# Performance work log

Measured on AMD Instinct MI355X. Metric: run time of the kernel, lower is better.

## Reference

```python
import jax, jax.numpy as jnp
import numpy as np

B, S, D, K = 64, 512, 512, 1024
DECAY = 0.99
EPS = 1e-05
COMMITMENT_COST = 0.25
PAD_IDX = 0


def setup_inputs() -> dict:
    key = jax.random.key(0)
    k1, k2, k3 = jax.random.split(key, 3)
    inputs = jax.random.normal(k1, (B, S, D), dtype=jnp.float32)
    padding_mask = jax.random.bernoulli(k2, 0.1, (B, S))
    codebook_w = jax.random.normal(k3, (K, D), dtype=jnp.float32) * 0.02
    codebook_w = codebook_w.at[PAD_IDX].set(0.0)  # padding_idx row zeroed
    ema_cluster_size = jnp.zeros((K,), dtype=jnp.float32)
    ema_w = codebook_w  # _ema_w initialized as copy of codebook
    return {"inputs": inputs, "padding_mask": padding_mask,
            "codebook_w": codebook_w, "ema_cluster_size": ema_cluster_size,
            "ema_w": ema_w}


def reference(inputs, padding_mask, codebook_w, ema_cluster_size, ema_w):
    input_shape = inputs.shape
    flat = inputs.reshape(-1, D)                      # [N, D]
    mask = padding_mask.reshape(-1)                   # [N], True = pad

    # squared euclidean distances: [N, K]
    dist = (jnp.sum(flat * flat, axis=1, keepdims=True)
            + jnp.sum(codebook_w * codebook_w, axis=1)
            - 2.0 * flat @ codebook_w.T)
    # non-padded tokens cannot pick code 0; padded tokens must pick code 0
    inf = jnp.float32(np.inf)
    col0 = jnp.where(mask, dist[:, 0], inf)
    rest = jnp.where(mask[:, None], inf, dist[:, 1:])
    dist = jnp.concatenate([col0[:, None], rest], axis=1)

    idx = jnp.argmin(dist, axis=1)                    # [N] int
    quantized = codebook_w[idx].reshape(input_shape)  # gather == onehot @ W

    num_nonpad = jnp.sum(~mask).astype(jnp.float32) * D
    e_latent_loss = jnp.sum((jax.lax.stop_gradient(quantized) - inputs) ** 2) / num_nonpad
    loss = COMMITMENT_COST * e_latent_loss

    # EMA codebook update (training branch, discard_ema_cluster_sizes=False)
    counts = jax.ops.segment_sum(jnp.ones_like(idx, dtype=jnp.float32), idx,
                                 num_segments=K)      # sum(encodings, 0)
    dw = jax.ops.segment_sum(flat, idx, num_segments=K)  # encodings.T @ flat
    cs = ema_cluster_size * DECAY + (1.0 - DECAY) * counts
    n = jnp.sum(cs)
    cs = (cs + EPS) / (n + K * EPS) * n
    new_ema_w = ema_w * DECAY + (1.0 - DECAY) * dw
    new_codebook = new_ema_w / cs[:, None]
    new_codebook = new_codebook.at[PAD_IDX].set(0.0)

    # straight-through estimator
    quantized_st = inputs + jax.lax.stop_gradient(quantized - inputs)

    avg_probs = counts / counts.shape[0] / (flat.shape[0] / K) if False else counts / flat.shape[0]
    perplexity = jnp.exp(-jnp.sum(avg_probs * jnp.log(avg_probs + 1e-10)))

    return (quantized_st, idx.reshape(input_shape[:-1]), loss, perplexity,
            cs, new_ema_w, new_codebook)
```

## Files before the change

kernel.cpp:

```cpp
#include <hip/hip_runtime.h>
#include <math.h>

#define N_TOK 32768
#define DDIM  512
#define KCODE 1024
#define DECAYF 0.99f
#define EPSV 1e-5f
#define CCOST 0.25f
#define MARGIN 0.02f
#define RT 8

typedef float f32x4 __attribute__((ext_vector_type(4)));
typedef short short8v __attribute__((ext_vector_type(8)));

__device__ __forceinline__ unsigned short f2bf(float f) {
  unsigned u = __float_as_uint(f);
  u += 0x7fffu + ((u >> 16) & 1u);
  return (unsigned short)(u >> 16);
}
__device__ __forceinline__ float bf2f(unsigned short h) {
  return __uint_as_float(((unsigned)h) << 16);
}

__device__ __forceinline__ unsigned ordf(float f) {
  unsigned u = __float_as_uint(f);
  return (u & 0x80000000u) ? ~u : (u | 0x80000000u);
}
__device__ __forceinline__ float ord2f(unsigned v) {
  unsigned u = (v & 0x80000000u) ? (v & 0x7fffffffu) : ~v;
  return __uint_as_float(u);
}
__device__ __forceinline__ void top2m(unsigned long long& a1, unsigned long long& a2,
                                      unsigned long long b1, unsigned long long b2) {
  unsigned long long m1 = a1 < b1 ? a1 : b1;
  unsigned long long hi = a1 < b1 ? b1 : a1;
  unsigned long long m2 = a2 < b2 ? a2 : b2;
  a2 = m2 < hi ? m2 : hi;
  a1 = m1;
}

__device__ __forceinline__ void stage16(const void* g, char* lds_base, int lane) {
#if __has_builtin(__builtin_amdgcn_global_load_lds)
  __builtin_amdgcn_global_load_lds((const __attribute__((address_space(1))) void*)g,
                                   (__attribute__((address_space(3))) void*)lds_base,
                                   16, 0, 0);
#else
  *(float4*)(lds_base + lane * 16) = *(const float4*)g;
#endif
}

__global__ __launch_bounds__(256) void convert_fused(
    const float* __restrict__ x, const float* __restrict__ w,
    unsigned short* __restrict__ xhi, unsigned short* __restrict__ whi,
    float* __restrict__ wn)
{
  int b = blockIdx.x;
  int tid = threadIdx.x;
  if (b < 16384) {
    size_t i = (size_t)b * 256 + tid;
    float4 v = *(const float4*)(x + i * 4);
    ushort4 h;
    h.x = f2bf(v.x);
    h.y = f2bf(v.y);
    h.z = f2bf(v.z);
    h.w = f2bf(v.w);
    *(ushort4*)(xhi + i * 4) = h;
  } else {
    int k = (b - 16384) * 4 + (tid >> 6);
    int lane = tid & 63;
    double s = 0.0;
    #pragma unroll
    for (int it = 0; it < 2; it++) {
      size_t off = (size_t)k * DDIM + (lane + 64 * it) * 4;
      float4 v = *(const float4*)(w + off);
      s += (double)v.x*(double)v.x + (double)v.y*(double)v.y
         + (double)v.z*(double)v.z + (double)v.w*(double)v.w;
      ushort4 h;
      h.x = f2bf(v.x);
      h.y = f2bf(v.y);
      h.z = f2bf(v.z);
      h.w = f2bf(v.w);
      *(ushort4*)(whi + off) = h;
    }
    for (int o = 32; o > 0; o >>= 1) s += __shfl_down(s, o, 64);
    if (lane == 0) wn[k] = (float)s;
  }
}

__global__ __launch_bounds__(256) void dist_mfma(
    const unsigned short* __restrict__ xhi, const unsigned short* __restrict__ whi,
    const float* __restrict__ wn,
    unsigned long long* __restrict__ k1buf, unsigned long long* __restrict__ k2buf)
{
  __shared__ __align__(16) short sA[128 * 32];
  __shared__ __align__(16) short sB[128 * 32];
  const int tid = threadIdx.x;
  const int wv = tid >> 6, lane = tid & 63;
  const int wg = (blockIdx.x & 7) * 256 + (blockIdx.x >> 3);
  const int tb = wg >> 3, kb = wg & 7;
  const int row0 = tb * 128, col0 = kb * 128;
  const int rw = wv & 1, cw = wv >> 1;
  const int q = lane >> 4, cl = lane & 15;
  const int swz = (cl >> 1) & 3;

  f32x4 acc[4][4];
  #pragma unroll
  for (int mt = 0; mt < 4; mt++)
    #pragma unroll
    for (int nt = 0; nt < 4; nt++) acc[mt][nt] = (f32x4){0.f, 0.f, 0.f, 0.f};

  const int cA0 = wv * 64 + lane;
  const int r0 = cA0 >> 2;
  const int s0 = (cA0 & 3) ^ ((r0 >> 1) & 3);
  const size_t aoff0 = (size_t)(row0 + r0) * 1024 + (size_t)s0 * 16;
  const size_t boff0 = (size_t)(col0 + r0) * 1024 + (size_t)s0 * 16;
  const char* pxh = (const char*)xhi;
  const char* pwh = (const char*)whi;

  const int aidx = (rw * 64 + cl) * 32 + (q ^ swz) * 8;
  const int bidx = (cw * 64 + cl) * 32 + (q ^ swz) * 8;

  for (int ks = 0; ks < 16; ks++) {
    const int k2 = ks * 64;
    __syncthreads();
    stage16(pxh + aoff0 + k2,         (char*)sA + wv * 1024, lane);
    stage16(pxh + aoff0 + 65536 + k2, (char*)sA + (wv + 4) * 1024, lane);
    stage16(pwh + boff0 + k2,         (char*)sB + wv * 1024, lane);
    stage16(pwh + boff0 + 65536 + k2, (char*)sB + (wv + 4) * 1024, lane);
    __syncthreads();

    short8v a[4], b[4];
    #pragma unroll
    for (int mt = 0; mt < 4; mt++) a[mt] = *(const short8v*)(sA + aidx + mt * 512);
    #pragma unroll
    for (int nt = 0; nt < 4; nt++) b[nt] = *(const short8v*)(sB + bidx + nt * 512);
    #pragma unroll
    for (int mt = 0; mt < 4; mt++)
      #pragma unroll
      for (int nt = 0; nt < 4; nt++)
        acc[mt][nt] = __builtin_amdgcn_mfma_f32_16x16x32_bf16(a[mt], b[nt], acc[mt][nt], 0, 0, 0);
  }

  float wnv[4];
  #pragma unroll
  for (int nt = 0; nt < 4; nt++) wnv[nt] = wn[col0 + cw * 64 + nt * 16 + cl];

  const int strip = kb * 2 + cw;
  #pragma unroll
  for (int mt = 0; mt < 4; mt++) {
    #pragma unroll
    for (int r = 0; r < 4; r++) {
      unsigned long long k1 = ~0ull, k2 = ~0ull;
      #pragma unroll
      for (int nt = 0; nt < 4; nt++) {
        int kk = col0 + cw * 64 + nt * 16 + cl;
        float dist = fmaf(-2.f, acc[mt][nt][r], wnv[nt]);
        unsigned long long key = (kk == 0) ? ~0ull
            : ((unsigned long long)ordf(dist) << 32) | (unsigned)kk;
        if (key < k1) { k2 = k1; k1 = key; }
        else if (key < k2) k2 = key;
      }
      #pragma unroll
      for (int off = 8; off > 0; off >>= 1) {
        unsigned long long o1 = __shfl_down(k1, off, 16);
        unsigned long long o2 = __shfl_down(k2, off, 16);
        top2m(k1, k2, o1, o2);
      }
      if (cl == 0) {
        int rowg = row0 + rw * 64 + mt * 16 + q * 4 + r;
        k1buf[strip * N_TOK + rowg] = k1;
        k2buf[strip * N_TOK + rowg] = k2;
      }
    }
  }
}

__global__ __launch_bounds__(1024) void combine_kernel(
    const unsigned long long* __restrict__ k1buf, const unsigned long long* __restrict__ k2buf,
    const int* __restrict__ mask,
    int* __restrict__ idx_i, int* __restrict__ flagList, int* __restrict__ flagcnt,
    int* __restrict__ counts_i)
{
  __shared__ int lh[KCODE];
  int tid = threadIdx.x;
  lh[tid] = 0;
  __syncthreads();
  int t = blockIdx.x * 1024 + tid;
  unsigned long long a1 = ~0ull, a2 = ~0ull;
  #pragma unroll
  for (int s = 0; s < 16; s++)
    top2m(a1, a2, k1buf[s * N_TOK + t], k2buf[s * N_TOK + t]);
  int bi = (int)(a1 & 0xffffffffu);
  float d1 = ord2f((unsigned)(a1 >> 32));
  float d2 = ord2f((unsigned)(a2 >> 32));
  int pad = mask[t];
  int id = pad ? 0 : bi;
  idx_i[t] = id;
  atomicAdd(&lh[id], 1);
  if (!pad && (d2 - d1) < MARGIN) {
    int p = atomicAdd(flagcnt, 1);
    flagList[p] = t;
  }
  __syncthreads();
  if (lh[tid] > 0) atomicAdd(&counts_i[tid], lh[tid]);
}

__global__ __launch_bounds__(256) void refine_kernel(
    const float* __restrict__ x, const float* __restrict__ w,
    const float* __restrict__ wn32,
    const int* __restrict__ flagList, const int* __restrict__ flagcnt,
    unsigned long long* __restrict__ keyMin)
{
  __shared__ double xd[RT][DDIM];
  __shared__ float  a32[RT];
  __shared__ unsigned long long wred[4][RT];
  int tid = threadIdx.x;
  int lane = tid & 63, wid = tid >> 6;
  int nf = *flagcnt;
  int nu = ((nf + RT - 1) / RT) * 4;
  for (int u = blockIdx.x; u < nu; u += gridDim.x) {
    int fi0 = (u >> 2) * RT;
    int qq = u & 3;
    #pragma unroll
    for (int tt = 0; tt < 2; tt++) {
      int ts = wid * 2 + tt;
      int fi = fi0 + ts;
      if (fi < nf) {
        int token = flagList[fi];
        double s = 0.0;
        #pragma unroll
        for (int it = 0; it < 2; it++) {
          int e4 = lane + it * 64;
          float4 v = *(const float4*)(x + (size_t)token * DDIM + e4 * 4);
          double vx = (double)v.x, vy = (double)v.y, vz = (double)v.z, vw = (double)v.w;
          xd[ts][e4 * 4 + 0] = vx;
          xd[ts][e4 * 4 + 1] = vy;
          xd[ts][e4 * 4 + 2] = vz;
          xd[ts][e4 * 4 + 3] = vw;
          s += vx * vx + vy * vy + vz * vz + vw * vw;
        }
        for (int o = 32; o > 0; o >>= 1) s += __shfl_down(s, o, 64);
        if (lane == 0) a32[ts] = (float)s;
      } else {
        #pragma unroll
        for (int it = 0; it < 2; it++) {
          int e4 = lane + it * 64;
          xd[ts][e4 * 4 + 0] = 0.0; xd[ts][e4 * 4 + 1] = 0.0;
          xd[ts][e4 * 4 + 2] = 0.0; xd[ts][e4 * 4 + 3] = 0.0;
        }
        if (lane == 0) a32[ts] = 0.f;
      }
    }
    __syncthreads();

    unsigned long long key[RT];
    #pragma unroll
    for (int t = 0; t < RT; t++) key[t] = ~0ull;
    int k = qq * 256 + tid;
    if (k != 0) {
      const float4* wr = (const float4*)(w + (size_t)k * DDIM);
      double dacc[RT];
      #pragma unroll
      for (int t = 0; t < RT; t++) dacc[t] = 0.0;
      float4 wv = wr[0];
      for (int dq = 0; dq < DDIM / 4; dq++) {
        float4 cv = wv;
        if (dq < DDIM / 4 - 1) wv = wr[dq + 1];
        double wx = (double)cv.x, wy = (double)cv.y, wz = (double)cv.z, ww2 = (double)cv.w;
        #pragma unroll
        for (int t = 0; t < RT; t++) {
          dacc[t] += xd[t][dq*4+0]*wx + xd[t][dq*4+1]*wy
                   + xd[t][dq*4+2]*wz + xd[t][dq*4+3]*ww2;
        }
      }
      float wnk = wn32[k];
      #pragma unroll
      for (int t = 0; t < RT; t++) {
        float M = (float)dacc[t];
        float AB = a32[t] + wnk;
        float dist = AB - 2.0f * M;
        key[t] = ((unsigned long long)ordf(dist) << 32) | (unsigned)k;
      }
    }

    #pragma unroll
    for (int t = 0; t < RT; t++) {
      unsigned long long kk = key[t];
      for (int o = 32; o > 0; o >>= 1) {
        unsigned long long ok = __shfl_down(kk, o, 64);
        if (ok < kk) kk = ok;
      }
      if (lane == 0) wred[wid][t] = kk;
    }
    __syncthreads();
    if (tid < RT) {
      int fi = fi0 + tid;
      if (fi < nf) {
        unsigned long long kk = wred[0][tid];
        if (wred[1][tid] < kk) kk = wred[1][tid];
        if (wred[2][tid] < kk) kk = wred[2][tid];
        if (wred[3][tid] < kk) kk = wred[3][tid];
        if (kk != ~0ull) atomicMin(&keyMin[fi], kk);
      }
    }
    __syncthreads();
  }
}

__global__ __launch_bounds__(256) void finalize_kernel(
    const int* __restrict__ flagList, const int* __restrict__ flagcnt,
    unsigned long long* __restrict__ keyMin,
    int* __restrict__ idx_i, int* __restrict__ counts_i)
{
  int fi = blockIdx.x * 256 + threadIdx.x;
  int nf = *flagcnt;
  if (fi < nf) {
    unsigned long long kk = keyMin[fi];
    int token = flagList[fi];
    int nw = (int)(kk & 0xffffffffu);
    int old = idx_i[token];
    if (nw != old) {
      idx_i[token] = nw;
      atomicSub(&counts_i[old], 1);
      atomicAdd(&counts_i[nw], 1);
    }
  }
  keyMin[fi] = 0ull;
}

__global__ __launch_bounds__(1024) void scan_kernel(
    const int* __restrict__ counts_i, int* __restrict__ offsets, int* __restrict__ cursor)
{
  __shared__ int tmp[1024];
  int t = threadIdx.x;
  int c = counts_i[t];
  tmp[t] = c;
  __syncthreads();
  for (int off = 1; off < 1024; off <<= 1) {
    int v = (t >= off) ? tmp[t - off] : 0;
    __syncthreads();
    tmp[t] += v;
    __syncthreads();
  }
  int ex = tmp[t] - c;
  offsets[t] = ex;
  cursor[t] = ex;
}

__global__ __launch_bounds__(1024) void scatter_kernel(
    const int* __restrict__ idx_i, int* __restrict__ cursor, int* __restrict__ bucket)
{
  __shared__ int lh[KCODE];
  __shared__ int lb[KCODE];
  int tid = threadIdx.x;
  lh[tid] = 0;
  __syncthreads();
  int token = blockIdx.x * 1024 + tid;
  int id = idx_i[token];
  int r = atomicAdd(&lh[id], 1);
  __syncthreads();
  if (lh[tid] > 0) lb[tid] = atomicAdd(&cursor[tid], lh[tid]);
  __syncthreads();
  bucket[lb[id] + r] = token;
}

__global__ __launch_bounds__(256) void quant_kernel(
    const float* __restrict__ x, const float* __restrict__ w,
    const int* __restrict__ idx_i,
    float* __restrict__ out_q, float* __restrict__ out_idx, float* __restrict__ losssum)
{
  __shared__ float sred[4];
  int tid = threadIdx.x;
  int qd = tid & 127, h = tid >> 7;
  float s = 0.f;
  #pragma unroll
  for (int i = 0; i < 8; i++) {
    int token = blockIdx.x * 16 + i * 2 + h;
    int idx = idx_i[token];
    float4 xv = *(const float4*)(x + (size_t)token * DDIM + qd * 4);
    float4 wv = *(const float4*)(w + (size_t)idx * DDIM + qd * 4);
    *(float4*)(out_q + (size_t)token * DDIM + qd * 4) = wv;
    if (qd == 0) out_idx[token] = (float)idx;
    float dx = wv.x - xv.x, dy = wv.y - xv.y, dz = wv.z - xv.z, dww = wv.w - xv.w;
    s += dx*dx + dy*dy + dz*dz + dww*dww;
  }
  for (int o = 32; o > 0; o >>= 1) s += __shfl_down(s, o, 64);
  int lane = tid & 63, wid = tid >> 6;
  if (lane == 0) sred[wid] = s;
  __syncthreads();
  if (tid == 0) atomicAdd(losssum, sred[0] + sred[1] + sred[2] + sred[3]);
}

__global__ __launch_bounds__(128) void dw_kernel(
    const float* __restrict__ x, const int* __restrict__ bucket,
    const int* __restrict__ idx_i, float* __restrict__ dw)
{
  int b0 = blockIdx.x * 32;
  int t = threadIdx.x;
  int ent = bucket[b0 + (t & 31)];
  int eid = idx_i[ent];
  int tok0 = __shfl(ent, 0, 64);
  int cur  = __shfl(eid, 0, 64);
  float4 acc = make_float4(0.f, 0.f, 0.f, 0.f);
  float4 nv = *(const float4*)(x + (size_t)tok0 * DDIM + t * 4);
  for (int j = 0; j < 32; j++) {
    float4 v = nv;
    int id = __shfl(eid, j, 64);
    if (j < 31) {
      int tn = __shfl(ent, j + 1, 64);
      nv = *(const float4*)(x + (size_t)tn * DDIM + t * 4);
    }
    if (id != cur) {
      float* p = dw + (size_t)cur * DDIM + t * 4;
      atomicAdd(p + 0, acc.x); atomicAdd(p + 1, acc.y);
      atomicAdd(p + 2, acc.z); atomicAdd(p + 3, acc.w);
      acc = make_float4(0.f, 0.f, 0.f, 0.f);
      cur = id;
    }
    acc.x += v.x; acc.y += v.y; acc.z += v.z; acc.w += v.w;
  }
  float* p = dw + (size_t)cur * DDIM + t * 4;
  atomicAdd(p + 0, acc.x); atomicAdd(p + 1, acc.y);
  atomicAdd(p + 2, acc.z); atomicAdd(p + 3, acc.w);
}

__global__ __launch_bounds__(1024) void stats_kernel(
    const int* __restrict__ counts_i, const float* __restrict__ ema_cs,
    const float* __restrict__ losssum,
    float* __restrict__ out_loss, float* __restrict__ out_perp,
    float* __restrict__ out_cs)
{
  __shared__ float sbuf[17];
  int k = threadIdx.x;
  float cnt = (float)counts_i[k];
  float csr = ema_cs[k] * DECAYF + (1.f - DECAYF) * cnt;
  float v = csr;
  for (int o = 32; o > 0; o >>= 1) v += __shfl_down(v, o, 64);
  int lane = k & 63, wid = k >> 6;
  if (lane == 0) sbuf[wid] = v;
  __syncthreads();
  if (k == 0) { float n = 0.f; for (int i = 0; i < 16; i++) n += sbuf[i]; sbuf[16] = n; }
  __syncthreads();
  float n = sbuf[16];
  out_cs[k] = (csr + EPSV) / (n + (float)KCODE * EPSV) * n;
  __syncthreads();
  float p = cnt / (float)N_TOK;
  v = p * logf(p + 1e-10f);
  for (int o = 32; o > 0; o >>= 1) v += __shfl_down(v, o, 64);
  if (lane == 0) sbuf[wid] = v;
  __syncthreads();
  if (k == 0) {
    float s = 0.f; for (int i = 0; i < 16; i++) s += sbuf[i];
    out_perp[0] = expf(-s);
    float nonpad = (float)(N_TOK - counts_i[0]);
    out_loss[0] = CCOST * losssum[0] / (nonpad * (float)DDIM);
  }
}

__global__ __launch_bounds__(256) void ema_kernel(
    const float* __restrict__ ema_w, const float* __restrict__ dw,
    const float* __restrict__ cs,
    float* __restrict__ out_ema, float* __restrict__ out_cb)
{
  int i = blockIdx.x * 256 + threadIdx.x;
  int e = i * 4;
  int k = e >> 9;
  float4 dv = *(const float4*)(dw + e);
  float4 ew = *(const float4*)(ema_w + e);
  float4 ne;
  ne.x = ew.x * DECAYF + (1.f - DECAYF) * dv.x;
  ne.y = ew.y * DECAYF + (1.f - DECAYF) * dv.y;
  ne.z = ew.z * DECAYF + (1.f - DECAYF) * dv.z;
  ne.w = ew.w * DECAYF + (1.f - DECAYF) * dv.w;
  *(float4*)(out_ema + e) = ne;
  float4 cb;
  if (k == 0) { cb.x = 0.f; cb.y = 0.f; cb.z = 0.f; cb.w = 0.f; }
  else {
    float csk = cs[k];
    cb.x = ne.x / csk; cb.y = ne.y / csk; cb.z = ne.z / csk; cb.w = ne.w / csk;
  }
  *(float4*)(out_cb + e) = cb;
}

extern "C" void kernel_launch(void* const* d_in, const int* in_sizes, int n_in,
                              void* d_out, int out_size, void* d_ws, size_t ws_size,
                              hipStream_t stream) {
  const float* x      = (const float*)d_in[0];
  const int*   mask   = (const int*)d_in[1];
  const float* w      = (const float*)d_in[2];
  const float* ema_cs = (const float*)d_in[3];
  const float* ema_w  = (const float*)d_in[4];
  float* out = (float*)d_out;

  float* out_q    = out;
  float* out_idx  = out + 16777216;
  float* out_loss = out + 16809984;
  float* out_perp = out + 16809985;
  float* out_cs   = out + 16809986;
  float* out_ema  = out + 16811010;
  float* out_cb   = out + 17335298;

  unsigned short* xhi = (unsigned short*)out_q;

  char* ws = (char*)d_ws;
  int*   counts_i = (int*)  (ws + 0);
  float* dw       = (float*)(ws + 4096);
  unsigned long long* keyMin = (unsigned long long*)(ws + 4096);
  float* losssum  = (float*)(ws + 2101248);
  int*   flagcnt  = (int*)  (ws + 2101252);
  int*   offsets  = (int*)  (ws + 2101312);
  int*   cursor   = (int*)  (ws + 2105408);
  float* wn       = (float*)(ws + 2109504);
  int*   idx_i    = (int*)  (ws + 2113600);
  int*   bucket   = (int*)  (ws + 2244672);
  unsigned short* whi = (unsigned short*)(ws + 2375744);
  unsigned long long* k1buf = (unsigned long long*)(ws + 4472896);
  unsigned long long* k2buf = (unsigned long long*)(ws + 8667200);
  int*   flagList = (int*)  (ws + 12861504);

  hipMemsetAsync(ws, 0, 2101256, stream);
  hipMemsetAsync(ws + 4096, 0xFF, 262144, stream);
  convert_fused<<<16384 + 256, 256, 0, stream>>>(x, w, xhi, whi, wn);
  dist_mfma<<<(N_TOK / 128) * 8, 256, 0, stream>>>(xhi, whi, wn, k1buf, k2buf);
  combine_kernel<<<N_TOK / 1024, 1024, 0, stream>>>(k1buf, k2buf, mask, idx_i, flagList, flagcnt, counts_i);
  refine_kernel<<<2048, 256, 0, stream>>>(x, w, wn, flagList, flagcnt, keyMin);
  finalize_kernel<<<N_TOK / 256 / 1, 256, 0, stream>>>(flagList, flagcnt, keyMin, idx_i, counts_i);
  scan_kernel<<<1, 1024, 0, stream>>>(counts_i, offsets, cursor);
  scatter_kernel<<<N_TOK / 1024, 1024, 0, stream>>>(idx_i, cursor, bucket);
  quant_kernel<<<N_TOK / 16, 256, 0, stream>>>(x, w, idx_i, out_q, out_idx, losssum);
  dw_kernel<<<N_TOK / 32, 128, 0, stream>>>(x, bucket, idx_i, dw);
  stats_kernel<<<1, 1024, 0, stream>>>(counts_i, ema_cs, losssum, out_loss, out_perp, out_cs);
  ema_kernel<<<KCODE * DDIM / 4 / 256, 256, 0, stream>>>(ema_w, dw, out_cs, out_ema, out_cb);
}
```

Before: 432.5 us.

## Add split-bf16 MFMA refinement stage before exact fp64 refine

Adds a middle refinement tier. Tokens flagged by the coarse bf16 pass are re-scored with a three-term hi/lo bf16 MFMA GEMM, which gives near-fp32 accuracy. Only tokens whose top-2 gap falls below a much tighter margin go on to the slow fp64 refine kernel. This adds writing lo-part arrays for x and W during conversion, plus an extra GEMM and combine launch. In exchange it aims to cut the costly scalar refine work.

After: 378.7 us. 12.4% less time.

```diff
diff --git a/kernel.cpp b/kernel.cpp
--- a/kernel.cpp
+++ b/kernel.cpp
@@ -8,6 +8,7 @@
 #define EPSV 1e-5f
 #define CCOST 0.25f
 #define MARGIN 0.02f
+#define MARGIN2 1e-3f
 #define RT 8
 
 typedef float f32x4 __attribute__((ext_vector_type(4)));
@@ -51,7 +52,8 @@
 
 __global__ __launch_bounds__(256) void convert_fused(
     const float* __restrict__ x, const float* __restrict__ w,
-    unsigned short* __restrict__ xhi, unsigned short* __restrict__ whi,
+    unsigned short* __restrict__ xhi, unsigned short* __restrict__ xlo,
+    unsigned short* __restrict__ whi, unsigned short* __restrict__ wlo,
     float* __restrict__ wn)
 {
   int b = blockIdx.x;
@@ -59,12 +61,13 @@
   if (b < 16384) {
     size_t i = (size_t)b * 256 + tid;
     float4 v = *(const float4*)(x + i * 4);
-    ushort4 h;
-    h.x = f2bf(v.x);
-    h.y = f2bf(v.y);
-    h.z = f2bf(v.z);
-    h.w = f2bf(v.w);
+    ushort4 h, l;
+    h.x = f2bf(v.x); l.x = f2bf(v.x - bf2f(h.x));
+    h.y = f2bf(v.y); l.y = f2bf(v.y - bf2f(h.y));
+    h.z = f2bf(v.z); l.z = f2bf(v.z - bf2f(h.z));
+    h.w = f2bf(v.w); l.w = f2bf(v.w - bf2f(h.w));
     *(ushort4*)(xhi + i * 4) = h;
+    *(ushort4*)(xlo + i * 4) = l;
   } else {
     int k = (b - 16384) * 4 + (tid >> 6);
     int lane = tid & 63;
@@ -75,12 +78,13 @@
       float4 v = *(const float4*)(w + off);
       s += (double)v.x*(double)v.x + (double)v.y*(double)v.y
          + (double)v.z*(double)v.z + (double)v.w*(double)v.w;
-      ushort4 h;
-      h.x = f2bf(v.x);
-      h.y = f2bf(v.y);
-      h.z = f2bf(v.z);
-      h.w = f2bf(v.w);
+      ushort4 h, l;
+      h.x = f2bf(v.x); l.x = f2bf(v.x - bf2f(h.x));
+      h.y = f2bf(v.y); l.y = f2bf(v.y - bf2f(h.y));
+      h.z = f2bf(v.z); l.z = f2bf(v.z - bf2f(h.z));
+      h.w = f2bf(v.w); l.w = f2bf(v.w - bf2f(h.w));
       *(ushort4*)(whi + off) = h;
+      *(ushort4*)(wlo + off) = l;
     }
     for (int o = 32; o > 0; o >>= 1) s += __shfl_down(s, o, 64);
     if (lane == 0) wn[k] = (float)s;
@@ -203,6 +207,158 @@
   }
   __syncthreads();
   if (lh[tid] > 0) atomicAdd(&counts_i[tid], lh[tid]);
+}
+
+__global__ __launch_bounds__(256) void refine_mfma(
+    const unsigned short* __restrict__ xhi, const unsigned short* __restrict__ xlo,
+    const unsigned short* __restrict__ whi, const unsigned short* __restrict__ wlo,
+    const float* __restrict__ wn,
+    const int* __restrict__ flagList, const int* __restrict__ flagcnt,
+    unsigned long long* __restrict__ k1buf, unsigned long long* __restrict__ k2buf)
+{
+  __shared__ __align__(16) short sAh[128 * 32];
+  __shared__ __align__(16) short sAl[128 * 32];
+  __shared__ __align__(16) short sBh[128 * 32];
+  __shared__ __align__(16) short sBl[128 * 32];
+  const int nf = *flagcnt;
+  const int tb = blockIdx.x >> 3, kb = blockIdx.x & 7;
+  const int fi0 = tb * 128;
+  if (fi0 >= nf) return;
+  const int tid = threadIdx.x;
+  const int wv = tid >> 6, lane = tid & 63;
+  const int col0 = kb * 128;
+  const int rw = wv & 1, cw = wv >> 1;
+  const int q = lane >> 4, cl = lane & 15;
+  const int swz = (cl >> 1) & 3;
+
+  f32x4 acc[4][4];
+  #pragma unroll
+  for (int mt = 0; mt < 4; mt++)
+    #pragma unroll
+    for (int nt = 0; nt < 4; nt++) acc[mt][nt] = (f32x4){0.f, 0.f, 0.f, 0.f};
+
+  const int cA0 = wv * 64 + lane;
+  const int r0 = cA0 >> 2;
+  const int s0 = (cA0 & 3) ^ ((r0 >> 1) & 3);
+  int fiA0 = fi0 + r0;      if (fiA0 > nf - 1) fiA0 = nf - 1;
+  int fiA1 = fi0 + r0 + 64; if (fiA1 > nf - 1) fiA1 = nf - 1;
+  const int tokA0 = flagList[fiA0];
+  const int tokA1 = flagList[fiA1];
+  const size_t aoff0 = (size_t)tokA0 * 1024 + (size_t)s0 * 16;
+  const size_t aoff1 = (size_t)tokA1 * 1024 + (size_t)s0 * 16;
+  const size_t boff0 = (size_t)(col0 + r0) * 1024 + (size_t)s0 * 16;
+  const char* pxh = (const char*)xhi;
+  const char* pxl = (const char*)xlo;
+  const char* pwh = (const char*)whi;
+  const char* pwl = (const char*)wlo;
+
+  const int aidx = (rw * 64 + cl) * 32 + (q ^ swz) * 8;
+  const int bidx = (cw * 64 + cl) * 32 + (q ^ swz) * 8;
+
+  for (int ks = 0; ks < 16; ks++) {
+    const int k2o = ks * 64;
+    __syncthreads();
+    stage16(pxh + aoff0 + k2o,         (char*)sAh + wv * 1024, lane);
+    stage16(pxh + aoff1 + k2o,         (char*)sAh + (wv + 4) * 1024, lane);
+    stage16(pxl + aoff0 + k2o,         (char*)sAl + wv * 1024, lane);
+    stage16(pxl + aoff1 + k2o,         (char*)sAl + (wv + 4) * 1024, lane);
+    stage16(pwh + boff0 + k2o,         (char*)sBh + wv * 1024, lane);
+    stage16(pwh + boff0 + 65536 + k2o, (char*)sBh + (wv + 4) * 1024, lane);
+    stage16(pwl + boff0 + k2o,         (char*)sBl + wv * 1024, lane);
+    stage16(pwl + boff0 + 65536 + k2o, (char*)sBl + (wv + 4) * 1024, lane);
+    __syncthreads();
+
+    short8v ah[4], bh[4];
+    #pragma unroll
+    for (int mt = 0; mt < 4; mt++) ah[mt] = *(const short8v*)(sAh + aidx + mt * 512);
+    #pragma unroll
+    for (int nt = 0; nt < 4; nt++) bh[nt] = *(const short8v*)(sBh + bidx + nt * 512);
+    #pragma unroll
+    for (int mt = 0; mt < 4; mt++)
+      #pragma unroll
+      for (int nt = 0; nt < 4; nt++)
+        acc[mt][nt] = __builtin_amdgcn_mfma_f32_16x16x32_bf16(ah[mt], bh[nt], acc[mt][nt], 0, 0, 0);
+
+    short8v bl[4];
+    #pragma unroll
+    for (int nt = 0; nt < 4; nt++) bl[nt] = *(const short8v*)(sBl + bidx + nt * 512);
+    #pragma unroll
+    for (int mt = 0; mt < 4; mt++)
+      #pragma unroll
+      for (int nt = 0; nt < 4; nt++)
+        acc[mt][nt] = __builtin_amdgcn_mfma_f32_16x16x32_bf16(ah[mt], bl[nt], acc[mt][nt], 0, 0, 0);
+
+    short8v al[4];
+    #pragma unroll
+    for (int mt = 0; mt < 4; mt++) al[mt] = *(const short8v*)(sAl + aidx + mt * 512);
+    #pragma unroll
+    for (int mt = 0; mt < 4; mt++)
+      #pragma unroll
+      for (int nt = 0; nt < 4; nt++)
+        acc[mt][nt] = __builtin_amdgcn_mfma_f32_16x16x32_bf16(al[mt], bh[nt], acc[mt][nt], 0, 0, 0);
+  }
+
+  float wnv[4];
+  #pragma unroll
+  for (int nt = 0; nt < 4; nt++) wnv[nt] = wn[col0 + cw * 64 + nt * 16 + cl];
+
+  const int strip = kb * 2 + cw;
+  #pragma unroll
+  for (int mt = 0; mt < 4; mt++) {
+    #pragma unroll
+    for (int r = 0; r < 4; r++) {
+      unsigned long long k1 = ~0ull, k2 = ~0ull;
+      #pragma unroll
+      for (int nt = 0; nt < 4; nt++) {
+        int kk = col0 + cw * 64 + nt * 16 + cl;
+        float dist = fmaf(-2.f, acc[mt][nt][r], wnv[nt]);
+        unsigned long long key = (kk == 0) ? ~0ull
+            : ((unsigned long long)ordf(dist) << 32) | (unsigned)kk;
+        if (key < k1) { k2 = k1; k1 = key; }
+        else if (key < k2) k2 = key;
+      }
+      #pragma unroll
+      for (int off = 8; off > 0; off >>= 1) {
+        unsigned long long o1 = __shfl_down(k1, off, 16);
+        unsigned long long o2 = __shfl_down(k2, off, 16);
+        top2m(k1, k2, o1, o2);
+      }
+      if (cl == 0) {
+        int fig = fi0 + rw * 64 + mt * 16 + q * 4 + r;
+        k1buf[strip * N_TOK + fig] = k1;
+        k2buf[strip * N_TOK + fig] = k2;
+      }
+    }
+  }
+}
+
+__global__ __launch_bounds__(256) void combine2_kernel(
+    const unsigned long long* __restrict__ k1buf, const unsigned long long* __restrict__ k2buf,
+    const int* __restrict__ flagList, const int* __restrict__ flagcnt,
+    int* __restrict__ idx_i, int* __restrict__ counts_i,
+    int* __restrict__ flagList2, int* __restrict__ flagcnt2)
+{
+  int fi = blockIdx.x * 256 + threadIdx.x;
+  int nf = *flagcnt;
+  if (fi >= nf) return;
+  unsigned long long a1 = ~0ull, a2 = ~0ull;
+  #pragma unroll
+  for (int s = 0; s < 16; s++)
+    top2m(a1, a2, k1buf[s * N_TOK + fi], k2buf[s * N_TOK + fi]);
+  int token = flagList[fi];
+  int nw = (int)(a1 & 0xffffffffu);
+  float d1 = ord2f((unsigned)(a1 >> 32));
+  float d2 = ord2f((unsigned)(a2 >> 32));
+  int old = idx_i[token];
+  if (nw != old) {
+    idx_i[token] = nw;
+    atomicSub(&counts_i[old], 1);
+    atomicAdd(&counts_i[nw], 1);
+  }
+  if ((d2 - d1) < MARGIN2) {
+    int p = atomicAdd(flagcnt2, 1);
+    flagList2[p] = token;
+  }
 }
 
 __global__ __launch_bounds__(256) void refine_kernel(
@@ -501,6 +657,7 @@
   float* out_cb   = out + 17335298;
 
   unsigned short* xhi = (unsigned short*)out_q;
+  unsigned short* xlo = xhi + (size_t)N_TOK * DDIM;
 
   char* ws = (char*)d_ws;
   int*   counts_i = (int*)  (ws + 0);
@@ -508,23 +665,28 @@
   unsigned long long* keyMin = (unsigned long long*)(ws + 4096);
   float* losssum  = (float*)(ws + 2101248);
   int*   flagcnt  = (int*)  (ws + 2101252);
+  int*   flagcnt2 = (int*)  (ws + 2101256);
   int*   offsets  = (int*)  (ws + 2101312);
   int*   cursor   = (int*)  (ws + 2105408);
   float* wn       = (float*)(ws + 2109504);
   int*   idx_i    = (int*)  (ws + 2113600);
   int*   bucket   = (int*)  (ws + 2244672);
   unsigned short* whi = (unsigned short*)(ws + 2375744);
+  unsigned short* wlo = (unsigned short*)(ws + 3424320);
   unsigned long long* k1buf = (unsigned long long*)(ws + 4472896);
   unsigned long long* k2buf = (unsigned long long*)(ws + 8667200);
-  int*   flagList = (int*)  (ws + 12861504);
-
-  hipMemsetAsync(ws, 0, 2101256, stream);
+  int*   flagList  = (int*) (ws + 12861504);
+  int*   flagList2 = (int*) (ws + 12992576);
+
+  hipMemsetAsync(ws, 0, 2101260, stream);
   hipMemsetAsync(ws + 4096, 0xFF, 262144, stream);
-  convert_fused<<<16384 + 256, 256, 0, stream>>>(x, w, xhi, whi, wn);
+  convert_fused<<<16384 + 256, 256, 0, stream>>>(x, w, xhi, xlo, whi, wlo, wn);
   dist_mfma<<<(N_TOK / 128) * 8, 256, 0, stream>>>(xhi, whi, wn, k1buf, k2buf);
   combine_kernel<<<N_TOK / 1024, 1024, 0, stream>>>(k1buf, k2buf, mask, idx_i, flagList, flagcnt, counts_i);
-  refine_kernel<<<2048, 256, 0, stream>>>(x, w, wn, flagList, flagcnt, keyMin);
-  finalize_kernel<<<N_TOK / 256 / 1, 256, 0, stream>>>(flagList, flagcnt, keyMin, idx_i, counts_i);
+  refine_mfma<<<(N_TOK / 128) * 8, 256, 0, stream>>>(xhi, xlo, whi, wlo, wn, flagList, flagcnt, k1buf, k2buf);
+  combine2_kernel<<<N_TOK / 256, 256, 0, stream>>>(k1buf, k2buf, flagList, flagcnt, idx_i, counts_i, flagList2, flagcnt2);
+  refine_kernel<<<2048, 256, 0, stream>>>(x, w, wn, flagList2, flagcnt2, keyMin);
+  finalize_kernel<<<N_TOK / 256, 256, 0, stream>>>(flagList2, flagcnt2, keyMin, idx_i, counts_i);
   scan_kernel<<<1, 1024, 0, stream>>>(counts_i, offsets, cursor);
   scatter_kernel<<<N_TOK / 1024, 1024, 0, stream>>>(idx_i, cursor, bucket);
   quant_kernel<<<N_TOK / 16, 256, 0, stream>>>(x, w, idx_i, out_q, out_idx, losssum);
```
